# Performance work log

Hardware: AMD Instinct MI355X
Metric: run time of the kernel (lower is better)

Reference implementation:

```python
import jax, jax.numpy as jnp
import numpy as np

B, H, S, Dh = 4, 16, 2048, 64
NEG = -1.0e9


def setup_inputs() -> dict:
    key = jax.random.key(0)
    kq, kk, kv = jax.random.split(key, 3)
    q = jax.random.normal(kq, (B, H, S, Dh), dtype=jnp.float32)
    k = jax.random.normal(kk, (B, H, S, Dh), dtype=jnp.float32)
    v = jax.random.normal(kv, (B, H, S, Dh), dtype=jnp.float32)
    # causal mask: 1.0 where attention is disallowed (j > i), matching mask * -1e9
    mask = jnp.triu(jnp.ones((S, S), dtype=jnp.float32), k=1)[None, None, :, :]
    return {"q": q, "k": k, "v": v, "mask": mask}


def reference(q, k, v, mask):
    # scaled dot-product attention: softmax(QK^T / sqrt(Dh) + mask * -1e9) V
    dim_k = jnp.asarray(k.shape[-1], dtype=jnp.float32)
    logits = jnp.einsum("bhsd,bhtd->bhst", q, k) / jnp.sqrt(dim_k)
    logits = logits + mask * NEG
    weights = jax.nn.softmax(logits, axis=-1)
    return jnp.einsum("bhst,bhtd->bhsd", weights, v)
```

## Files before the change

### kernel.cpp

```cpp
#include <hip/hip_runtime.h>

#define S_LEN 2048
#define DH 64

typedef float f32x4 __attribute__((ext_vector_type(4)));
typedef __bf16 bf16x8 __attribute__((ext_vector_type(8)));
typedef unsigned u32x2v __attribute__((ext_vector_type(2)));

#define MFMA16(A, B, C) __builtin_amdgcn_mfma_f32_16x16x32_bf16(A, B, C, 0, 0, 0)

#ifdef __has_builtin
#if __has_builtin(__builtin_amdgcn_permlane16_swap) && __has_builtin(__builtin_amdgcn_permlane32_swap)
#define HAVE_PLSWAP 1
#endif
#if __has_builtin(__builtin_amdgcn_global_load_lds)
#define HAVE_GLDS 1
#endif
#endif
#ifndef HAVE_PLSWAP
#define HAVE_PLSWAP 0
#endif
#ifndef HAVE_GLDS
#define HAVE_GLDS 0
#endif

__device__ __forceinline__ unsigned short f2bf(float f) {
    unsigned u = __builtin_bit_cast(unsigned, f);
    u += 0x7fffu + ((u >> 16) & 1u);
    return (unsigned short)(u >> 16);
}

__device__ __forceinline__ uint4 pack8(const float* s) {
    unsigned short h[8];
#pragma unroll
    for (int i = 0; i < 8; ++i) h[i] = f2bf(s[i]);
    return *(const uint4*)h;
}

__device__ __forceinline__ unsigned pack_tr(float a, float b) {
    return __builtin_amdgcn_perm(__builtin_bit_cast(unsigned, b),
                                 __builtin_bit_cast(unsigned, a), 0x07060302u);
}

__device__ __forceinline__ bf16x8 ld128(const unsigned short* p) {
    return __builtin_bit_cast(bf16x8, *(const uint4*)p);
}

__device__ __forceinline__ bf16x8 ones8() {
    uint4 ou; ou.x = 0x3F803F80u; ou.y = ou.x; ou.z = ou.x; ou.w = ou.x;
    return __builtin_bit_cast(bf16x8, ou);
}

__device__ __forceinline__ void pl32pair(unsigned& x, unsigned& y) {
#if HAVE_PLSWAP
    u32x2v r = __builtin_amdgcn_permlane32_swap(x, y, false, false);
    x = r[0]; y = r[1];
#else
    unsigned sx = __shfl_xor(x, 32, 64);
    unsigned sy = __shfl_xor(y, 32, 64);
    const bool hi = (threadIdx.x & 32) != 0;
    unsigned nx = hi ? sy : x;
    unsigned ny = hi ? y : sx;
    x = nx; y = ny;
#endif
}

__device__ __forceinline__ void pl16pair(unsigned& x, unsigned& y) {
#if HAVE_PLSWAP
    u32x2v r = __builtin_amdgcn_permlane16_swap(x, y, false, false);
    x = r[0]; y = r[1];
#else
    unsigned sx = __shfl_xor(x, 16, 64);
    unsigned sy = __shfl_xor(y, 16, 64);
    const bool odd = (threadIdx.x & 16) != 0;
    unsigned nx = odd ? sy : x;
    unsigned ny = odd ? y : sx;
    x = nx; y = ny;
#endif
}

__device__ __forceinline__ bf16x8 frag_from(unsigned A0, unsigned B0,
                                            unsigned A1, unsigned B1) {
    pl32pair(A0, A1);
    pl16pair(A0, A1);
    pl32pair(B0, B1);
    pl16pair(B0, B1);
    uint4 u; u.x = A0; u.y = B0; u.z = A1; u.w = B1;
    return __builtin_bit_cast(bf16x8, u);
}

__device__ __forceinline__ void glds16(const uint4* g, unsigned short* l) {
#if HAVE_GLDS
    __builtin_amdgcn_global_load_lds(
        (const __attribute__((address_space(1))) uint4*)g,
        (__attribute__((address_space(3))) uint4*)l, 16, 0, 0);
#else
    *(uint4*)l = *g;
#endif
}

__global__ __launch_bounds__(256) void prep_kv(const float* __restrict__ k,
                                               const float* __restrict__ v,
                                               uint4* __restrict__ kimg,
                                               uint4* __restrict__ vimg) {
    __shared__ unsigned short tr[64 * 40];
    const int bid = blockIdx.x;
    const int t = threadIdx.x;
    if (bid < 4096) {
        const int r = t >> 3, b = t & 7;
        const int srcblk = b ^ (r & 7);
        const float* src = k + ((size_t)bid * 32 + r) * 64 + srcblk * 8;
        float buf[8];
        *(float4*)&buf[0] = *(const float4*)src;
        *(float4*)&buf[4] = *(const float4*)(src + 4);
        kimg[(size_t)bid * 256 + t] = pack8(buf);
    } else {
        const int vb = bid - 4096;
        const int r = t >> 3, cb = t & 7;
        const float* src = v + ((size_t)vb * 32 + r) * 64 + cb * 8;
        float buf[8];
        *(float4*)&buf[0] = *(const float4*)src;
        *(float4*)&buf[4] = *(const float4*)(src + 4);
#pragma unroll
        for (int i = 0; i < 8; ++i)
            tr[(cb * 8 + i) * 40 + r] = f2bf(buf[i]);
        __syncthreads();
        const int d = t >> 2, kb = t & 3;
        const int skb = kb ^ ((d >> 1) & 3);
        vimg[(size_t)vb * 256 + t] = *(const uint4*)&tr[d * 40 + skb * 8];
    }
}

template <bool MA, bool MB, bool LB, bool SHARED>
__device__ __forceinline__ void body2(
    const unsigned short* __restrict__ ktA, const unsigned short* __restrict__ vtA,
    const unsigned short* __restrict__ ktB, const unsigned short* __restrict__ vtB,
    const bf16x8* qA, const bf16x8* qB,
    f32x4* accA, f32x4* accB, f32x4& aclA, f32x4& aclB,
    int igA, int igB, int kbA, int kbB, int quad, int c)
{
    const int sw = c & 7;
    const bf16x8 ones = ones8();
    const int f0 = (quad ^ sw) << 3;
    const int f1 = ((quad | 4) ^ sw) << 3;
    bf16x8 pfA[2], pfB[2];
#pragma unroll
    for (int h = 0; h < 2; ++h) {
        unsigned pA[2][2], pB[2][2];
#pragma unroll
        for (int m = 0; m < 2; ++m) {
            const int mt = 2 * h + m;
            const unsigned short* krA = ktA + (mt * 16 + c) * 64;
            bf16x8 kA0 = ld128(krA + f0), kA1 = ld128(krA + f1);
            {
                f32x4 s = (f32x4){0.f, 0.f, 0.f, 0.f};
                s = MFMA16(kA0, qA[0], s);
                s = MFMA16(kA1, qA[1], s);
                float p[4];
#pragma unroll
                for (int r = 0; r < 4; ++r) {
                    float e = __builtin_amdgcn_exp2f(s[r]);
                    if (MA) {
                        const int jg = kbA + mt * 16 + quad * 4 + r;
                        e = (jg > igA) ? 0.f : e;
                    }
                    p[r] = e;
                }
                pA[m][0] = pack_tr(p[0], p[1]);
                pA[m][1] = pack_tr(p[2], p[3]);
            }
            if (LB) {
                bf16x8 kB0, kB1;
                if (SHARED) { kB0 = kA0; kB1 = kA1; }
                else {
                    const unsigned short* krB = ktB + (mt * 16 + c) * 64;
                    kB0 = ld128(krB + f0); kB1 = ld128(krB + f1);
                }
                f32x4 s = (f32x4){0.f, 0.f, 0.f, 0.f};
                s = MFMA16(kB0, qB[0], s);
                s = MFMA16(kB1, qB[1], s);
                float p[4];
#pragma unroll
                for (int r = 0; r < 4; ++r) {
                    float e = __builtin_amdgcn_exp2f(s[r]);
                    if (MB) {
                        const int jg = kbB + mt * 16 + quad * 4 + r;
                        e = (jg > igB) ? 0.f : e;
                    }
                    p[r] = e;
                }
                pB[m][0] = pack_tr(p[0], p[1]);
                pB[m][1] = pack_tr(p[2], p[3]);
            }
        }
        pfA[h] = frag_from(pA[0][0], pA[0][1], pA[1][0], pA[1][1]);
        aclA = MFMA16(pfA[h], ones, aclA);
        if (LB) {
            pfB[h] = frag_from(pB[0][0], pB[0][1], pB[1][0], pB[1][1]);
            aclB = MFMA16(pfB[h], ones, aclB);
        }
    }
    const int vsw = (c >> 1) & 3;
#pragma unroll
    for (int dc = 0; dc < 4; ++dc) {
        const int vo = (dc * 16 + c) * 32 + ((quad ^ vsw) << 3);
        bf16x8 v0 = ld128(vtA + vo), v1 = ld128(vtA + vo + 2048);
        accA[dc] = MFMA16(pfA[0], v0, accA[dc]);
        accA[dc] = MFMA16(pfA[1], v1, accA[dc]);
        if (LB) {
            bf16x8 w0, w1;
            if (SHARED) { w0 = v0; w1 = v1; }
            else { w0 = ld128(vtB + vo); w1 = ld128(vtB + vo + 2048); }
            accB[dc] = MFMA16(pfB[0], w0, accB[dc]);
            accB[dc] = MFMA16(pfB[1], w1, accB[dc]);
        }
    }
}

__device__ __forceinline__ void write_strip(float* __restrict__ ob,
                                            const f32x4* acc, const f32x4 acl,
                                            int rowbase, int quad, int c) {
    float linv[4];
#pragma unroll
    for (int r = 0; r < 4; ++r) linv[r] = 1.0f / acl[r];
#pragma unroll
    for (int dc = 0; dc < 4; ++dc)
#pragma unroll
        for (int r = 0; r < 4; ++r) {
            const size_t idx =
                (size_t)(rowbase + quad * 4 + r) * DH + dc * 16 + c;
            ob[idx] = acc[dc][r] * linv[r];
        }
}

__global__ __launch_bounds__(256, 4) void fa_kernel(
    const float* __restrict__ q,
    const uint4* __restrict__ kimg,
    const uint4* __restrict__ vimg,
    float* __restrict__ out)
{
    __shared__ unsigned short kt[2][64 * 64];
    __shared__ unsigned short vt[2][2 * 64 * 32];

    const int tid  = threadIdx.x;
    const int lane = tid & 63;
    const int wave = tid >> 6;
    const int quad = lane >> 4;
    const int c    = lane & 15;

    const int bid = blockIdx.x;
    const int bh  = bid & 63;
    const int ci  = bid >> 6;
    const int hib = (31 - ci) * 64 + wave * 16;
    const int lob = ci * 64 + wave * 16;

    const size_t head_off = (size_t)bh * S_LEN * DH;

    const uint4* kin = kimg + (size_t)bh * 16384;
    const uint4* vin = vimg + (size_t)bh * 16384;

    auto stage = [&](int jt, int b) {
        const uint4* kg = kin + jt * 512 + tid;
        const uint4* vg = vin + jt * 512 + tid;
        glds16(kg,       &kt[b][0] + (size_t)tid * 8);
        glds16(kg + 256, &kt[b][0] + (size_t)(tid + 256) * 8);
        glds16(vg,       &vt[b][0] + (size_t)tid * 8);
        glds16(vg + 256, &vt[b][0] + (size_t)(tid + 256) * 8);
    };

    stage(0, 0);

    const float SCALE = 0.125f * 1.4426950408889634f;
    bf16x8 qf[4];
#pragma unroll
    for (int s = 0; s < 2; ++s) {
        const int base = s ? lob : hib;
        const float* qrow = q + head_off + (size_t)(base + c) * DH;
        float t0[8], t1[8];
#pragma unroll
        for (int i = 0; i < 8; ++i) t0[i] = qrow[quad * 8 + i] * SCALE;
#pragma unroll
        for (int i = 0; i < 8; ++i) t1[i] = qrow[32 + quad * 8 + i] * SCALE;
        qf[s * 2 + 0] = __builtin_bit_cast(bf16x8, pack8(t0));
        qf[s * 2 + 1] = __builtin_bit_cast(bf16x8, pack8(t1));
    }

    f32x4 accA[4], accB[4];
#pragma unroll
    for (int dc = 0; dc < 4; ++dc) {
        accA[dc] = (f32x4){0.f, 0.f, 0.f, 0.f};
        accB[dc] = (f32x4){0.f, 0.f, 0.f, 0.f};
    }
    f32x4 aclA = (f32x4){0.f, 0.f, 0.f, 0.f};
    f32x4 aclB = (f32x4){0.f, 0.f, 0.f, 0.f};

    const int igA = hib + c;
    const int igB = lob + c;

    int cur = 0;
    for (int jt = 0; jt <= ci; ++jt) {
        __syncthreads();
        if (jt < ci) stage(jt + 1, cur ^ 1);
        const int kb = jt * 64;
        if (jt < ci)
            body2<false, false, true, true>(kt[cur], vt[cur], kt[cur], vt[cur],
                                            qf, qf + 2, accA, accB, aclA, aclB,
                                            igA, igB, kb, kb, quad, c);
        else
            body2<false, true, true, true>(kt[cur], vt[cur], kt[cur], vt[cur],
                                           qf, qf + 2, accA, accB, aclA, aclB,
                                           igA, igB, kb, kb, quad, c);
        cur ^= 1;
    }

    write_strip(out + head_off, accB, aclB, lob, quad, c);
#pragma unroll
    for (int dc = 0; dc < 4; ++dc) accB[dc] = (f32x4){0.f, 0.f, 0.f, 0.f};
    aclB = (f32x4){0.f, 0.f, 0.f, 0.f};

    for (int i = 0; i <= 15 - ci; ++i) {
        const int t0 = ci + 1 + 2 * i;
        const bool single = (t0 == 31 - ci);
        __syncthreads();
        stage(t0, 0);
        if (!single) stage(t0 + 1, 1);
        __syncthreads();
        if (single)
            body2<true, false, false, true>(kt[0], vt[0], kt[0], vt[0],
                                            qf, qf, accA, accB, aclA, aclB,
                                            igA, igA, t0 * 64, t0 * 64, quad, c);
        else
            body2<false, false, true, false>(kt[0], vt[0], kt[1], vt[1],
                                             qf, qf, accA, accB, aclA, aclB,
                                             igA, igA, t0 * 64, (t0 + 1) * 64,
                                             quad, c);
    }

#pragma unroll
    for (int dc = 0; dc < 4; ++dc) accA[dc] += accB[dc];
    aclA += aclB;
    write_strip(out + head_off, accA, aclA, hib, quad, c);
}

#define KT_STRIDE 88
#define VT_STRIDE 36
__global__ __launch_bounds__(256) void fa_kernel_fb(
    const float* __restrict__ q, const float* __restrict__ k,
    const float* __restrict__ v, float* __restrict__ out)
{
    __shared__ unsigned short kts[32 * KT_STRIDE];
    __shared__ unsigned short vts[64 * VT_STRIDE];
    __shared__ unsigned short pts[4][16 * 40];
    const int tid = threadIdx.x, lane = tid & 63, wave = tid >> 6;
    const int quad = lane >> 4, c = lane & 15;
    const int bid = blockIdx.x, bh = bid & 63, qblk = 31 - (bid >> 6);
    const int qtile = qblk * 4 + wave, qbase = qtile * 16;
    const int my_diag = qtile >> 1, jt_last = (qblk * 4 + 3) >> 1;
    const size_t head_off = (size_t)bh * S_LEN * DH;
    const float* qrow = q + head_off + (size_t)(qbase + c) * DH;
    float qtmp[8];
#pragma unroll
    for (int i = 0; i < 8; ++i) qtmp[i] = qrow[quad * 8 + i];
    bf16x8 qf0 = __builtin_bit_cast(bf16x8, pack8(qtmp));
#pragma unroll
    for (int i = 0; i < 8; ++i) qtmp[i] = qrow[32 + quad * 8 + i];
    bf16x8 qf1 = __builtin_bit_cast(bf16x8, pack8(qtmp));
    f32x4 acc[4];
#pragma unroll
    for (int dc = 0; dc < 4; ++dc) acc[dc] = (f32x4){0.f, 0.f, 0.f, 0.f};
    float m_run = -1e30f, l_run = 0.f;
    const int ig = qbase + c;
    const int srow = tid >> 3, sdb = tid & 7;
    const int vcol = (((srow >> 3) ^ (sdb & 3)) << 3) | (srow & 7);
    const float LOG2E = 1.4426950408889634f;
    for (int jt = 0; jt <= jt_last; ++jt) {
        __syncthreads();
        {
            const size_t g = head_off + (size_t)(jt * 32 + srow) * DH + sdb * 8;
            float kbuf[8];
            *(float4*)&kbuf[0] = *(const float4*)(k + g);
            *(float4*)&kbuf[4] = *(const float4*)(k + g + 4);
            *(uint4*)&kts[srow * KT_STRIDE + sdb * 8] = pack8(kbuf);
            float vbuf[8];
            *(float4*)&vbuf[0] = *(const float4*)(v + g);
            *(float4*)&vbuf[4] = *(const float4*)(v + g + 4);
#pragma unroll
            for (int i = 0; i < 8; ++i)
                vts[(sdb * 8 + i) * VT_STRIDE + vcol] = f2bf(vbuf[i]);
        }
        __syncthreads();
        if (jt > my_diag) continue;
        f32x4 st[2];
#pragma unroll
        for (int mt = 0; mt < 2; ++mt) {
            const unsigned short* krow = &kts[(mt * 16 + c) * KT_STRIDE + quad * 8];
            bf16x8 ka0 = __builtin_bit_cast(bf16x8, *(const uint4*)krow);
            bf16x8 ka1 = __builtin_bit_cast(bf16x8, *(const uint4*)(krow + 32));
            f32x4 a = (f32x4){0.f, 0.f, 0.f, 0.f};
            a = MFMA16(ka0, qf0, a);
            a = MFMA16(ka1, qf1, a);
            st[mt] = a;
        }
        float tv[8];
#pragma unroll
        for (int mt = 0; mt < 2; ++mt)
#pragma unroll
            for (int r = 0; r < 4; ++r) {
                const int jg = jt * 32 + mt * 16 + quad * 4 + r;
                const float s = st[mt][r] * 0.125f;
                tv[mt * 4 + r] = (jg > ig) ? -1e30f : s;
            }
        float tm = tv[0];
#pragma unroll
        for (int i = 1; i < 8; ++i) tm = fmaxf(tm, tv[i]);
        tm = fmaxf(tm, __shfl_xor(tm, 16, 64));
        tm = fmaxf(tm, __shfl_xor(tm, 32, 64));
        const float m_new = fmaxf(m_run, tm);
        const float mb = m_new * LOG2E;
        float p[8], ps = 0.f;
#pragma unroll
        for (int i = 0; i < 8; ++i) {
            p[i] = __builtin_amdgcn_exp2f(tv[i] * LOG2E - mb);
            ps += p[i];
        }
        ps += __shfl_xor(ps, 16, 64);
        ps += __shfl_xor(ps, 32, 64);
        const float alpha = __builtin_amdgcn_exp2f((m_run - m_new) * LOG2E);
        l_run = l_run * alpha + ps;
        m_run = m_new;
        unsigned short* pwf = pts[wave];
#pragma unroll
        for (int mt = 0; mt < 2; ++mt)
#pragma unroll
            for (int r = 0; r < 4; ++r)
                pwf[c * 40 + mt * 16 + quad * 4 + r] = f2bf(p[mt * 4 + r]);
        float ar[4];
#pragma unroll
        for (int r = 0; r < 4; ++r)
            ar[r] = __shfl(alpha, (quad << 4) + quad * 4 + r, 64);
#pragma unroll
        for (int dc = 0; dc < 4; ++dc)
#pragma unroll
            for (int r = 0; r < 4; ++r) acc[dc][r] *= ar[r];
        bf16x8 pf = __builtin_bit_cast(bf16x8, *(const uint4*)&pwf[c * 40 + quad * 8]);
#pragma unroll
        for (int dc = 0; dc < 4; ++dc) {
            const int vrow = dc * 16 + c;
            const int blk = quad ^ ((vrow >> 3) & 3);
            const unsigned short* vp = &vts[vrow * VT_STRIDE + blk * 8];
            uint2 a0 = *(const uint2*)vp;
            uint2 a1 = *(const uint2*)(vp + 4);
            uint4 u; u.x = a0.x; u.y = a0.y; u.z = a1.x; u.w = a1.y;
            bf16x8 vf = __builtin_bit_cast(bf16x8, u);
            acc[dc] = MFMA16(pf, vf, acc[dc]);
        }
    }
    float linv[4];
#pragma unroll
    for (int r = 0; r < 4; ++r) {
        const float lr = __shfl(l_run, (quad << 4) + quad * 4 + r, 64);
        linv[r] = 1.0f / lr;
    }
    float* ob = out + head_off;
#pragma unroll
    for (int dc = 0; dc < 4; ++dc)
#pragma unroll
        for (int r = 0; r < 4; ++r) {
            const size_t idx = (size_t)(qbase + quad * 4 + r) * DH + dc * 16 + c;
            ob[idx] = acc[dc][r] * linv[r];
        }
}

extern "C" void kernel_launch(void* const* d_in, const int* in_sizes, int n_in,
                              void* d_out, int out_size, void* d_ws, size_t ws_size,
                              hipStream_t stream) {
    const float* q = (const float*)d_in[0];
    const float* k = (const float*)d_in[1];
    const float* v = (const float*)d_in[2];
    float* o = (float*)d_out;
    const size_t need = (size_t)2 * 64 * 64 * 4096;
    if (ws_size >= need) {
        uint4* kimg = (uint4*)d_ws;
        uint4* vimg = kimg + (size_t)64 * 64 * 256;
        hipLaunchKernelGGL(prep_kv, dim3(8192), dim3(256), 0, stream, k, v, kimg, vimg);
        hipLaunchKernelGGL(fa_kernel, dim3(1024), dim3(256), 0, stream, q, kimg, vimg, o);
    } else {
        hipLaunchKernelGGL(fa_kernel_fb, dim3(2048), dim3(256), 0, stream, q, k, v, o);
    }
}
```

Before: 188.9 us.

## Pipeline second-phase KV tiles with double buffering and raise wave priority around MFMA

The second phase, where only the high query strip remains, used to load two K/V tiles, then synchronize, then compute, with no overlap between loads and math. It now runs one tile per iteration with the same prefetch-next-tile double buffering as the first phase. The first phase also prefetches across the boundary into the second. The work alternates between two accumulator sets via a new single-strip body1 helper. s_setprio is raised around the compute bodies to favour MFMA issue. The trade-off is more barrier iterations with less MFMA work per barrier.

```diff
diff --git a/kernel.cpp b/kernel.cpp
--- a/kernel.cpp
+++ b/kernel.cpp
@@ -16,12 +16,18 @@
 #if __has_builtin(__builtin_amdgcn_global_load_lds)
 #define HAVE_GLDS 1
 #endif
+#if __has_builtin(__builtin_amdgcn_s_setprio)
+#define SETPRIO(x) __builtin_amdgcn_s_setprio(x)
+#endif
 #endif
 #ifndef HAVE_PLSWAP
 #define HAVE_PLSWAP 0
 #endif
 #ifndef HAVE_GLDS
 #define HAVE_GLDS 0
+#endif
+#ifndef SETPRIO
+#define SETPRIO(x)
 #endif
 
 __device__ __forceinline__ unsigned short f2bf(float f) {
@@ -131,13 +137,12 @@
     }
 }
 
-template <bool MA, bool MB, bool LB, bool SHARED>
+template <bool MB>
 __device__ __forceinline__ void body2(
-    const unsigned short* __restrict__ ktA, const unsigned short* __restrict__ vtA,
-    const unsigned short* __restrict__ ktB, const unsigned short* __restrict__ vtB,
+    const unsigned short* __restrict__ kt_, const unsigned short* __restrict__ vt_,
     const bf16x8* qA, const bf16x8* qB,
-    f32x4* accA, f32x4* accB, f32x4& aclA, f32x4& aclB,
-    int igA, int igB, int kbA, int kbB, int quad, int c)
+    f32x4 (&accA)[4], f32x4 (&accB)[4], f32x4& aclA, f32x4& aclB,
+    int igB, int kb, int quad, int c)
 {
     const int sw = c & 7;
     const bf16x8 ones = ones8();
@@ -150,41 +155,28 @@
 #pragma unroll
         for (int m = 0; m < 2; ++m) {
             const int mt = 2 * h + m;
-            const unsigned short* krA = ktA + (mt * 16 + c) * 64;
-            bf16x8 kA0 = ld128(krA + f0), kA1 = ld128(krA + f1);
+            const unsigned short* kr = kt_ + (mt * 16 + c) * 64;
+            bf16x8 k0 = ld128(kr + f0), k1 = ld128(kr + f1);
             {
                 f32x4 s = (f32x4){0.f, 0.f, 0.f, 0.f};
-                s = MFMA16(kA0, qA[0], s);
-                s = MFMA16(kA1, qA[1], s);
+                s = MFMA16(k0, qA[0], s);
+                s = MFMA16(k1, qA[1], s);
                 float p[4];
 #pragma unroll
-                for (int r = 0; r < 4; ++r) {
-                    float e = __builtin_amdgcn_exp2f(s[r]);
-                    if (MA) {
-                        const int jg = kbA + mt * 16 + quad * 4 + r;
-                        e = (jg > igA) ? 0.f : e;
-                    }
-                    p[r] = e;
-                }
+                for (int r = 0; r < 4; ++r) p[r] = __builtin_amdgcn_exp2f(s[r]);
                 pA[m][0] = pack_tr(p[0], p[1]);
                 pA[m][1] = pack_tr(p[2], p[3]);
             }
-            if (LB) {
-                bf16x8 kB0, kB1;
-                if (SHARED) { kB0 = kA0; kB1 = kA1; }
-                else {
-                    const unsigned short* krB = ktB + (mt * 16 + c) * 64;
-                    kB0 = ld128(krB + f0); kB1 = ld128(krB + f1);
-                }
+            {
                 f32x4 s = (f32x4){0.f, 0.f, 0.f, 0.f};
-                s = MFMA16(kB0, qB[0], s);
-                s = MFMA16(kB1, qB[1], s);
+                s = MFMA16(k0, qB[0], s);
+                s = MFMA16(k1, qB[1], s);
                 float p[4];
 #pragma unroll
                 for (int r = 0; r < 4; ++r) {
                     float e = __builtin_amdgcn_exp2f(s[r]);
                     if (MB) {
-                        const int jg = kbB + mt * 16 + quad * 4 + r;
+                        const int jg = kb + mt * 16 + quad * 4 + r;
                         e = (jg > igB) ? 0.f : e;
                     }
                     p[r] = e;
@@ -195,25 +187,66 @@
         }
         pfA[h] = frag_from(pA[0][0], pA[0][1], pA[1][0], pA[1][1]);
         aclA = MFMA16(pfA[h], ones, aclA);
-        if (LB) {
-            pfB[h] = frag_from(pB[0][0], pB[0][1], pB[1][0], pB[1][1]);
-            aclB = MFMA16(pfB[h], ones, aclB);
-        }
+        pfB[h] = frag_from(pB[0][0], pB[0][1], pB[1][0], pB[1][1]);
+        aclB = MFMA16(pfB[h], ones, aclB);
     }
     const int vsw = (c >> 1) & 3;
 #pragma unroll
     for (int dc = 0; dc < 4; ++dc) {
         const int vo = (dc * 16 + c) * 32 + ((quad ^ vsw) << 3);
-        bf16x8 v0 = ld128(vtA + vo), v1 = ld128(vtA + vo + 2048);
+        bf16x8 v0 = ld128(vt_ + vo), v1 = ld128(vt_ + vo + 2048);
         accA[dc] = MFMA16(pfA[0], v0, accA[dc]);
         accA[dc] = MFMA16(pfA[1], v1, accA[dc]);
-        if (LB) {
-            bf16x8 w0, w1;
-            if (SHARED) { w0 = v0; w1 = v1; }
-            else { w0 = ld128(vtB + vo); w1 = ld128(vtB + vo + 2048); }
-            accB[dc] = MFMA16(pfB[0], w0, accB[dc]);
-            accB[dc] = MFMA16(pfB[1], w1, accB[dc]);
-        }
+        accB[dc] = MFMA16(pfB[0], v0, accB[dc]);
+        accB[dc] = MFMA16(pfB[1], v1, accB[dc]);
+    }
+}
+
+template <bool MASK>
+__device__ __forceinline__ void body1(
+    const unsigned short* __restrict__ kt_, const unsigned short* __restrict__ vt_,
+    const bf16x8* qA, f32x4 (&acc)[4], f32x4& acl,
+    int ig, int kb, int quad, int c)
+{
+    const int sw = c & 7;
+    const bf16x8 ones = ones8();
+    const int f0 = (quad ^ sw) << 3;
+    const int f1 = ((quad | 4) ^ sw) << 3;
+    bf16x8 pf[2];
+#pragma unroll
+    for (int h = 0; h < 2; ++h) {
+        unsigned pA[2][2];
+#pragma unroll
+        for (int m = 0; m < 2; ++m) {
+            const int mt = 2 * h + m;
+            const unsigned short* kr = kt_ + (mt * 16 + c) * 64;
+            bf16x8 k0 = ld128(kr + f0), k1 = ld128(kr + f1);
+            f32x4 s = (f32x4){0.f, 0.f, 0.f, 0.f};
+            s = MFMA16(k0, qA[0], s);
+            s = MFMA16(k1, qA[1], s);
+            float p[4];
+#pragma unroll
+            for (int r = 0; r < 4; ++r) {
+                float e = __builtin_amdgcn_exp2f(s[r]);
+                if (MASK) {
+                    const int jg = kb + mt * 16 + quad * 4 + r;
+                    e = (jg > ig) ? 0.f : e;
+                }
+                p[r] = e;
+            }
+            pA[m][0] = pack_tr(p[0], p[1]);
+            pA[m][1] = pack_tr(p[2], p[3]);
+        }
+        pf[h] = frag_from(pA[0][0], pA[0][1], pA[1][0], pA[1][1]);
+        acl = MFMA16(pf[h], ones, acl);
+    }
+    const int vsw = (c >> 1) & 3;
+#pragma unroll
+    for (int dc = 0; dc < 4; ++dc) {
+        const int vo = (dc * 16 + c) * 32 + ((quad ^ vsw) << 3);
+        bf16x8 v0 = ld128(vt_ + vo), v1 = ld128(vt_ + vo + 2048);
+        acc[dc] = MFMA16(pf[0], v0, acc[dc]);
+        acc[dc] = MFMA16(pf[1], v1, acc[dc]);
     }
 }
 
@@ -251,7 +284,8 @@
     const int bid = blockIdx.x;
     const int bh  = bid & 63;
     const int ci  = bid >> 6;
-    const int hib = (31 - ci) * 64 + wave * 16;
+    const int last = 31 - ci;
+    const int hib = last * 64 + wave * 16;
     const int lob = ci * 64 + wave * 16;
 
     const size_t head_off = (size_t)bh * S_LEN * DH;
@@ -297,20 +331,20 @@
     const int igA = hib + c;
     const int igB = lob + c;
 
-    int cur = 0;
-    for (int jt = 0; jt <= ci; ++jt) {
+    int jt = 0;
+    for (; jt <= ci; ++jt) {
         __syncthreads();
-        if (jt < ci) stage(jt + 1, cur ^ 1);
-        const int kb = jt * 64;
+        if (jt < last) stage(jt + 1, (jt + 1) & 1);
+        const unsigned short* K = kt[jt & 1];
+        const unsigned short* V = vt[jt & 1];
+        SETPRIO(1);
         if (jt < ci)
-            body2<false, false, true, true>(kt[cur], vt[cur], kt[cur], vt[cur],
-                                            qf, qf + 2, accA, accB, aclA, aclB,
-                                            igA, igB, kb, kb, quad, c);
+            body2<false>(K, V, qf, qf + 2, accA, accB, aclA, aclB,
+                         igB, jt * 64, quad, c);
         else
-            body2<false, true, true, true>(kt[cur], vt[cur], kt[cur], vt[cur],
-                                           qf, qf + 2, accA, accB, aclA, aclB,
-                                           igA, igB, kb, kb, quad, c);
-        cur ^= 1;
+            body2<true>(K, V, qf, qf + 2, accA, accB, aclA, aclB,
+                        igB, jt * 64, quad, c);
+        SETPRIO(0);
     }
 
     write_strip(out + head_off, accB, aclB, lob, quad, c);
@@ -318,22 +352,21 @@
     for (int dc = 0; dc < 4; ++dc) accB[dc] = (f32x4){0.f, 0.f, 0.f, 0.f};
     aclB = (f32x4){0.f, 0.f, 0.f, 0.f};
 
-    for (int i = 0; i <= 15 - ci; ++i) {
-        const int t0 = ci + 1 + 2 * i;
-        const bool single = (t0 == 31 - ci);
+    for (; jt <= last; ++jt) {
         __syncthreads();
-        stage(t0, 0);
-        if (!single) stage(t0 + 1, 1);
-        __syncthreads();
-        if (single)
-            body2<true, false, false, true>(kt[0], vt[0], kt[0], vt[0],
-                                            qf, qf, accA, accB, aclA, aclB,
-                                            igA, igA, t0 * 64, t0 * 64, quad, c);
-        else
-            body2<false, false, true, false>(kt[0], vt[0], kt[1], vt[1],
-                                             qf, qf, accA, accB, aclA, aclB,
-                                             igA, igA, t0 * 64, (t0 + 1) * 64,
-                                             quad, c);
+        if (jt < last) stage(jt + 1, (jt + 1) & 1);
+        const unsigned short* K = kt[jt & 1];
+        const unsigned short* V = vt[jt & 1];
+        const int kb = jt * 64;
+        SETPRIO(1);
+        if ((jt ^ ci) & 1) {
+            if (jt == last) body1<true >(K, V, qf, accB, aclB, igA, kb, quad, c);
+            else            body1<false>(K, V, qf, accB, aclB, igA, kb, quad, c);
+        } else {
+            if (jt == last) body1<true >(K, V, qf, accA, aclA, igA, kb, quad, c);
+            else            body1<false>(K, V, qf, accA, aclA, igA, kb, quad, c);
+        }
+        SETPRIO(0);
     }
 
 #pragma unroll
```

After: 187.1 us. Within noise of the previous version (-0.9%).
